# Kernel tuning notes

Measured on AMD Instinct MI355X. Metric: run time of the kernel, lower is better.

The kernel has to match this reference:

```python
import jax, jax.numpy as jnp
import numpy as np

N_NODES = 50000
N_EDGES = 600000
D = 128
L = 3


def setup_inputs() -> dict:
    key = jax.random.key(0)
    ks = jax.random.split(key, 6)
    x = jax.random.normal(ks[0], (N_NODES, D), dtype=jnp.float32)
    edge_index = jax.random.randint(ks[1], (2, N_EDGES), 0, N_NODES, dtype=jnp.int64)
    # Glorot-ish scale for 128x128 linears
    s = 1.0 / np.sqrt(D)
    W_l = jax.random.normal(ks[2], (L, D, D), dtype=jnp.float32) * s
    b_l = jnp.zeros((L, D), dtype=jnp.float32)
    W_r = jax.random.normal(ks[3], (L, D, D), dtype=jnp.float32) * s
    W_out = jax.random.normal(ks[4], (D, 1), dtype=jnp.float32) * s
    b_out = jnp.zeros((1,), dtype=jnp.float32)
    return {"x": x, "edge_index": edge_index, "W_l": W_l, "b_l": b_l,
            "W_r": W_r, "W_out": W_out, "b_out": b_out}


def reference(x, edge_index, W_l, b_l, W_r, W_out, b_out):
    # PyG SAGEConv (aggr='mean', root_weight=True):
    #   out_i = lin_l(mean_{j: (j->i)} x_j) + lin_r(x_i)
    src = edge_index[0]
    dst = edge_index[1]
    n = x.shape[0]
    deg = jax.ops.segment_sum(jnp.ones(src.shape, x.dtype), dst, num_segments=n)
    inv_deg = (1.0 / jnp.maximum(deg, 1.0))[:, None]  # [N,1]
    h = x
    for i in range(W_l.shape[0]):  # fixed small layer count
        agg = jax.ops.segment_sum(h[src], dst, num_segments=n) * inv_deg  # [N,D]
        h = agg @ W_l[i] + b_l[i] + h @ W_r[i]
        h = jax.nn.relu(h)  # dropout is identity at eval (p=0.0)
    return (h @ W_out + b_out)[:, 0]  # squeeze(-1) -> [N]
```

## Files before the change

### kernel.cpp

```cpp
#include <hip/hip_runtime.h>

#define N_NODES 50000
#define N_EDGES 600000
#define D 128
#define NLAYERS 3
#define ELL_W 64

typedef __attribute__((ext_vector_type(8))) short short8;
typedef __attribute__((ext_vector_type(4))) float floatx4;

__device__ __forceinline__ float bf_lo(unsigned u) { return __uint_as_float(u << 16); }
__device__ __forceinline__ float bf_hi(unsigned u) { return __uint_as_float(u & 0xffff0000u); }
__device__ __forceinline__ unsigned short f2bf(float f) {
    unsigned u = __float_as_uint(f);
    return (unsigned short)((u + 0x7fffu + ((u >> 16) & 1u)) >> 16);
}


#define SEC_A (N_NODES * D / 4)
#define SEC_B (SEC_A + NLAYERS * D * 256)
#define SEC_TOT (SEC_B + N_NODES)

__global__ void cvt_init_kernel(const float* __restrict__ x, const float* __restrict__ Wl,
                                const float* __restrict__ Wr,
                                unsigned short* __restrict__ xb,
                                unsigned short* __restrict__ hb1,
                                unsigned short* __restrict__ hb2,
                                unsigned short* __restrict__ WtF,
                                int* __restrict__ cursor) {
    int i = blockIdx.x * blockDim.x + threadIdx.x;
    if (i < SEC_A) {
        float4 v = ((const float4*)x)[i];
        ushort4 o;
        o.x = f2bf(v.x); o.y = f2bf(v.y); o.z = f2bf(v.z); o.w = f2bf(v.w);
        ((ushort4*)xb)[i] = o;
    } else if (i < SEC_B) {
        int t = i - SEC_A;
        int l = t >> 15;
        int r = t & 32767;
        int f = r >> 3;
        int ii = r & 7;
        int jkt = f >> 6;
        int lane = f & 63;
        int j = jkt >> 3;
        int kt = jkt & 7;
        int half = lane & 15;
        int quad = lane >> 4;
        int n = j * 16 + half;
        int k = kt * 32 + quad * 8 + ii;
        float v = (k < D) ? Wl[(size_t)l * D * D + (size_t)k * D + n]
                          : Wr[(size_t)l * D * D + (size_t)(k - D) * D + n];
        WtF[t] = f2bf(v);
    } else if (i < SEC_TOT) {
        int j = i - SEC_B;
        cursor[j] = 0;
        if (j < D) {
            xb[(size_t)N_NODES * D + j] = 0;
            hb1[(size_t)N_NODES * D + j] = 0;
            hb2[(size_t)N_NODES * D + j] = 0;
        }
    }
}


__global__ void fill_kernel(const int* __restrict__ src, const int* __restrict__ dst,
                            int* __restrict__ cursor, unsigned short* __restrict__ ell) {
    int e = blockIdx.x * blockDim.x + threadIdx.x;
    if (e < N_EDGES) {
        int d_ = dst[e];
        int pos = atomicAdd(&cursor[d_], 1);
        if (pos < ELL_W) ell[(size_t)d_ * ELL_W + pos] = (unsigned short)src[e];
    }
}


template <bool LAST>
__global__ __launch_bounds__(256) void fused_layer_kernel(
    const unsigned short* __restrict__ hin,
    const int* __restrict__ degc, const unsigned short* __restrict__ ell,
    const unsigned short* __restrict__ WtF, const float* __restrict__ bias,
    unsigned short* __restrict__ hout,
    const float* __restrict__ Wout, const float* __restrict__ bout,
    float* __restrict__ out) {
    __shared__ union {
        unsigned short a[32 * 256];
        unsigned short c[32][136];
        float red[32][4];
    } sh;

    int m0 = blockIdx.x * 32;
    int tid = threadIdx.x;

    uint4 st0, st1;
    int strow0, stcol0, strow1, stcol1;
    {
        int t0 = tid;
        strow0 = t0 >> 4; stcol0 = t0 & 15;
        int row0 = min(m0 + strow0, N_NODES - 1);
        st0 = *((const uint4*)(hin + (size_t)row0 * D + stcol0 * 8));
        int t1 = 256 + tid;
        strow1 = t1 >> 4; stcol1 = t1 & 15;
        int row1 = min(m0 + strow1, N_NODES - 1);
        st1 = *((const uint4*)(hin + (size_t)row1 * D + stcol1 * 8));
    }

    {
        int grp = tid >> 4;
        int q = tid & 15;
        int nodeA = m0 + grp;
        int nodeB = m0 + grp + 16;
        int dA = (nodeA < N_NODES) ? min(degc[nodeA], ELL_W) : 0;
        int dB = (nodeB < N_NODES) ? min(degc[nodeB], ELL_W) : 0;
        #pragma unroll
        for (int half_ = 0; half_ < 2; ++half_) {
            int nl = grp + half_ * 16;
            int node = m0 + nl;
            int d = half_ ? dB : dA;
            float a[8] = {0.f, 0.f, 0.f, 0.f, 0.f, 0.f, 0.f, 0.f};
            float b8[8] = {0.f, 0.f, 0.f, 0.f, 0.f, 0.f, 0.f, 0.f};
            float w = 0.f;
            if (node < N_NODES) {
                int pd = (d + 3) & ~3;
                int base = node * ELL_W;
                for (int e = 0; e < pd; e += 16) {
                    int cnt = min(pd - e, 16);
                    int idx = ell[base + e + q];
                    for (int j = 0; j < cnt; j += 4) {
                        int rem = d - e - j;
                        int s0 = __shfl(idx, j + 0, 16);
                        int s1 = __shfl(idx, j + 1, 16);
                        int s2 = __shfl(idx, j + 2, 16);
                        int s3 = __shfl(idx, j + 3, 16);
                        s1 = (1 < rem) ? s1 : N_NODES;
                        s2 = (2 < rem) ? s2 : N_NODES;
                        s3 = (3 < rem) ? s3 : N_NODES;
                        uint4 v0 = *((const uint4*)(hin + (size_t)s0 * D + q * 8));
                        uint4 v1 = *((const uint4*)(hin + (size_t)s1 * D + q * 8));
                        uint4 v2 = *((const uint4*)(hin + (size_t)s2 * D + q * 8));
                        uint4 v3 = *((const uint4*)(hin + (size_t)s3 * D + q * 8));
                        a[0] += bf_lo(v0.x); a[1] += bf_hi(v0.x);
                        a[2] += bf_lo(v0.y); a[3] += bf_hi(v0.y);
                        a[4] += bf_lo(v0.z); a[5] += bf_hi(v0.z);
                        a[6] += bf_lo(v0.w); a[7] += bf_hi(v0.w);
                        b8[0] += bf_lo(v1.x); b8[1] += bf_hi(v1.x);
                        b8[2] += bf_lo(v1.y); b8[3] += bf_hi(v1.y);
                        b8[4] += bf_lo(v1.z); b8[5] += bf_hi(v1.z);
                        b8[6] += bf_lo(v1.w); b8[7] += bf_hi(v1.w);
                        a[0] += bf_lo(v2.x); a[1] += bf_hi(v2.x);
                        a[2] += bf_lo(v2.y); a[3] += bf_hi(v2.y);
                        a[4] += bf_lo(v2.z); a[5] += bf_hi(v2.z);
                        a[6] += bf_lo(v2.w); a[7] += bf_hi(v2.w);
                        b8[0] += bf_lo(v3.x); b8[1] += bf_hi(v3.x);
                        b8[2] += bf_lo(v3.y); b8[3] += bf_hi(v3.y);
                        b8[4] += bf_lo(v3.z); b8[5] += bf_hi(v3.z);
                        b8[6] += bf_lo(v3.w); b8[7] += bf_hi(v3.w);
                    }
                }
                w = 1.0f / (float)max(d, 1);
            }
            uint4 o;
            o.x = (unsigned)f2bf((a[0] + b8[0]) * w) | ((unsigned)f2bf((a[1] + b8[1]) * w) << 16);
            o.y = (unsigned)f2bf((a[2] + b8[2]) * w) | ((unsigned)f2bf((a[3] + b8[3]) * w) << 16);
            o.z = (unsigned)f2bf((a[4] + b8[4]) * w) | ((unsigned)f2bf((a[5] + b8[5]) * w) << 16);
            o.w = (unsigned)f2bf((a[6] + b8[6]) * w) | ((unsigned)f2bf((a[7] + b8[7]) * w) << 16);
            int chunk = q ^ (nl & 7);
            *((uint4*)&sh.a[nl * 256 + chunk * 8]) = o;
        }
    }

    {
        int chunk0 = (16 + stcol0) ^ (strow0 & 7);
        *((uint4*)&sh.a[strow0 * 256 + chunk0 * 8]) = st0;
        int chunk1 = (16 + stcol1) ^ (strow1 & 7);
        *((uint4*)&sh.a[strow1 * 256 + chunk1 * 8]) = st1;
    }
    __syncthreads();

    int wv = tid >> 6;
    int lane = tid & 63;
    int half = lane & 15;
    int quad = lane >> 4;

    floatx4 acc[2][2];
    #pragma unroll
    for (int mt = 0; mt < 2; mt++)
        #pragma unroll
        for (int jj = 0; jj < 2; jj++)
            acc[mt][jj] = (floatx4){0.f, 0.f, 0.f, 0.f};

    const short8* Bf = (const short8*)WtF;
    #pragma unroll
    for (int kt = 0; kt < 8; kt++) {
        int ch = (kt * 4 + quad) ^ (half & 7);
        short8 a0 = *((const short8*)&sh.a[half * 256 + ch * 8]);
        short8 a1 = *((const short8*)&sh.a[(16 + half) * 256 + ch * 8]);
        #pragma unroll
        for (int jj = 0; jj < 2; jj++) {
            int j = wv * 2 + jj;
            short8 b = Bf[(j * 8 + kt) * 64 + lane];
            acc[0][jj] = __builtin_amdgcn_mfma_f32_16x16x32_bf16(a0, b, acc[0][jj], 0, 0, 0);
            acc[1][jj] = __builtin_amdgcn_mfma_f32_16x16x32_bf16(a1, b, acc[1][jj], 0, 0, 0);
        }
    }
    __syncthreads();

    if (!LAST) {
        #pragma unroll
        for (int jj = 0; jj < 2; jj++) {
            int col = (wv * 2 + jj) * 16 + half;
            float bv = bias[col];
            #pragma unroll
            for (int mt = 0; mt < 2; mt++)
                #pragma unroll
                for (int r = 0; r < 4; r++)
                    sh.c[mt * 16 + quad * 4 + r][col] = f2bf(fmaxf(acc[mt][jj][r] + bv, 0.f));
        }
        __syncthreads();
        #pragma unroll
        for (int it = 0; it < 2; ++it) {
            int t = it * 256 + tid;
            int rl = t >> 4;
            int c = t & 15;
            int row = m0 + rl;
            if (row < N_NODES)
                *((uint4*)(hout + (size_t)row * D + c * 8)) = *((const uint4*)&sh.c[rl][c * 8]);
        }
    } else {
        float vout[2][4] = {{0.f, 0.f, 0.f, 0.f}, {0.f, 0.f, 0.f, 0.f}};
        #pragma unroll
        for (int jj = 0; jj < 2; jj++) {
            int col = (wv * 2 + jj) * 16 + half;
            float bv = bias[col];
            float wo = Wout[col];
            #pragma unroll
            for (int mt = 0; mt < 2; mt++)
                #pragma unroll
                for (int r = 0; r < 4; r++)
                    vout[mt][r] += fmaxf(acc[mt][jj][r] + bv, 0.f) * wo;
        }
        #pragma unroll
        for (int off = 1; off < 16; off <<= 1) {
            #pragma unroll
            for (int mt = 0; mt < 2; mt++)
                #pragma unroll
                for (int r = 0; r < 4; r++)
                    vout[mt][r] += __shfl_xor(vout[mt][r], off, 64);
        }
        if (half == 0) {
            #pragma unroll
            for (int mt = 0; mt < 2; mt++)
                #pragma unroll
                for (int r = 0; r < 4; r++)
                    sh.red[mt * 16 + quad * 4 + r][wv] = vout[mt][r];
        }
        __syncthreads();
        if (tid < 32) {
            int row = m0 + tid;
            if (row < N_NODES)
                out[row] = sh.red[tid][0] + sh.red[tid][1] +
                           sh.red[tid][2] + sh.red[tid][3] + bout[0];
        }
    }
}


extern "C" void kernel_launch(void* const* d_in, const int* in_sizes, int n_in,
                              void* d_out, int out_size, void* d_ws, size_t ws_size,
                              hipStream_t stream) {
    const float* x     = (const float*)d_in[0];
    const int*   edge  = (const int*)d_in[1];
    const float* W_l   = (const float*)d_in[2];
    const float* b_l   = (const float*)d_in[3];
    const float* W_r   = (const float*)d_in[4];
    const float* W_out = (const float*)d_in[5];
    const float* b_out = (const float*)d_in[6];
    float* out = (float*)d_out;

    char* ws = (char*)d_ws;
    size_t off = 0;
    auto alloc = [&](size_t bytes) -> void* {
        void* p = ws + off;
        off += (bytes + 255) & ~(size_t)255;
        return p;
    };
    unsigned short* xb  = (unsigned short*)alloc((size_t)(N_NODES + 1) * D * 2);
    unsigned short* hb1 = (unsigned short*)alloc((size_t)(N_NODES + 1) * D * 2);
    unsigned short* hb2 = (unsigned short*)alloc((size_t)(N_NODES + 1) * D * 2);
    unsigned short* WtF = (unsigned short*)alloc((size_t)NLAYERS * D * 256 * 2);
    int* cursor = (int*)alloc((size_t)N_NODES * sizeof(int));
    unsigned short* ell = (unsigned short*)alloc((size_t)N_NODES * ELL_W * sizeof(unsigned short));

    const int* src = edge;
    const int* dst = edge + N_EDGES;

    cvt_init_kernel<<<(SEC_TOT + 255) / 256, 256, 0, stream>>>(
        x, W_l, W_r, xb, hb1, hb2, WtF, cursor);
    fill_kernel<<<(N_EDGES + 255) / 256, 256, 0, stream>>>(src, dst, cursor, ell);

    const int grid = (N_NODES + 31) / 32;

    fused_layer_kernel<false><<<grid, 256, 0, stream>>>(
        xb, cursor, ell, WtF, b_l, hb1, W_out, b_out, out);
    fused_layer_kernel<false><<<grid, 256, 0, stream>>>(
        hb1, cursor, ell, WtF + (size_t)1 * D * 256, b_l + 1 * D, hb2, W_out, b_out, out);
    fused_layer_kernel<true><<<grid, 256, 0, stream>>>(
        hb2, cursor, ell, WtF + (size_t)2 * D * 256, b_l + 2 * D, hb1, W_out, b_out, out);
}
```

Before: 207.4 us.

## Merge three layer launches into a persistent kernel with grid barriers

Replaces the three per-layer kernel launches with one persistent kernel of 1024 blocks. Each block loops over 32-row tiles, and the layers are separated by a software grid barrier built on atomic counters that the init kernel zeroes. The goal is to remove inter-kernel launch gaps and tail drain between layers. In exchange it adds barrier spin overhead and an uneven tile-to-block distribution. It also depends on all 1024 blocks being co-resident; if they are not, the barrier deadlocks.

```diff
diff --git a/kernel.cpp b/kernel.cpp
--- a/kernel.cpp
+++ b/kernel.cpp
@@ -5,6 +5,7 @@
 #define D 128
 #define NLAYERS 3
 #define ELL_W 64
+#define NBLK 1024
 
 typedef __attribute__((ext_vector_type(8))) short short8;
 typedef __attribute__((ext_vector_type(4))) float floatx4;
@@ -15,7 +16,6 @@
     unsigned u = __float_as_uint(f);
     return (unsigned short)((u + 0x7fffu + ((u >> 16) & 1u)) >> 16);
 }
-
 
 #define SEC_A (N_NODES * D / 4)
 #define SEC_B (SEC_A + NLAYERS * D * 256)
@@ -27,7 +27,7 @@
                                 unsigned short* __restrict__ hb1,
                                 unsigned short* __restrict__ hb2,
                                 unsigned short* __restrict__ WtF,
-                                int* __restrict__ cursor) {
+                                int* __restrict__ cursor, int* __restrict__ bar) {
     int i = blockIdx.x * blockDim.x + threadIdx.x;
     if (i < SEC_A) {
         float4 v = ((const float4*)x)[i];
@@ -54,6 +54,7 @@
     } else if (i < SEC_TOT) {
         int j = i - SEC_B;
         cursor[j] = 0;
+        if (j < 256) bar[j] = 0;
         if (j < D) {
             xb[(size_t)N_NODES * D + j] = 0;
             hb1[(size_t)N_NODES * D + j] = 0;
@@ -61,7 +62,6 @@
         }
     }
 }
-
 
 __global__ void fill_kernel(const int* __restrict__ src, const int* __restrict__ dst,
                             int* __restrict__ cursor, unsigned short* __restrict__ ell) {
@@ -73,22 +73,36 @@
     }
 }
 
+__device__ __forceinline__ void grid_barrier(int* bar, int nblk) {
+    __syncthreads();
+    if (threadIdx.x == 0) {
+        __threadfence();
+        int g = blockIdx.x & 7;
+        int v = atomicAdd(&bar[g * 16], 1) + 1;
+        if (v == (nblk >> 3)) atomicAdd(&bar[127], 1);
+        while (__hip_atomic_load(&bar[127], __ATOMIC_ACQUIRE,
+                                 __HIP_MEMORY_SCOPE_AGENT) < 8)
+            __builtin_amdgcn_s_sleep(16);
+        __threadfence();
+    }
+    __syncthreads();
+}
+
+union SharedU {
+    unsigned short a[32 * 256];
+    unsigned short c[32][136];
+    float red[32][4];
+};
 
 template <bool LAST>
-__global__ __launch_bounds__(256) void fused_layer_kernel(
+__device__ __forceinline__ void layer_tile(
+    SharedU& sh, int m0,
     const unsigned short* __restrict__ hin,
     const int* __restrict__ degc, const unsigned short* __restrict__ ell,
     const unsigned short* __restrict__ WtF, const float* __restrict__ bias,
     unsigned short* __restrict__ hout,
     const float* __restrict__ Wout, const float* __restrict__ bout,
     float* __restrict__ out) {
-    __shared__ union {
-        unsigned short a[32 * 256];
-        unsigned short c[32][136];
-        float red[32][4];
-    } sh;
-
-    int m0 = blockIdx.x * 32;
     int tid = threadIdx.x;
 
     uint4 st0, st1;
@@ -261,6 +275,29 @@
                            sh.red[tid][2] + sh.red[tid][3] + bout[0];
         }
     }
+    __syncthreads();
+}
+
+__global__ __launch_bounds__(256, 4) void persistent_layers_kernel(
+    const unsigned short* __restrict__ xb,
+    unsigned short* __restrict__ hb1, unsigned short* __restrict__ hb2,
+    const int* __restrict__ degc, const unsigned short* __restrict__ ell,
+    const unsigned short* __restrict__ WtF, const float* __restrict__ b_l,
+    const float* __restrict__ Wout, const float* __restrict__ bout,
+    float* __restrict__ out, int* __restrict__ bar) {
+    __shared__ SharedU sh;
+    const int NT = (N_NODES + 31) / 32;
+
+    for (int t = blockIdx.x; t < NT; t += gridDim.x)
+        layer_tile<false>(sh, t * 32, xb, degc, ell, WtF, b_l, hb1, Wout, bout, out);
+    grid_barrier(bar, gridDim.x);
+    for (int t = blockIdx.x; t < NT; t += gridDim.x)
+        layer_tile<false>(sh, t * 32, hb1, degc, ell, WtF + D * 256, b_l + D,
+                          hb2, Wout, bout, out);
+    grid_barrier(bar + 128, gridDim.x);
+    for (int t = blockIdx.x; t < NT; t += gridDim.x)
+        layer_tile<true>(sh, t * 32, hb2, degc, ell, WtF + 2 * D * 256, b_l + 2 * D,
+                         hb1, Wout, bout, out);
 }
 
 
@@ -289,20 +326,14 @@
     unsigned short* WtF = (unsigned short*)alloc((size_t)NLAYERS * D * 256 * 2);
     int* cursor = (int*)alloc((size_t)N_NODES * sizeof(int));
     unsigned short* ell = (unsigned short*)alloc((size_t)N_NODES * ELL_W * sizeof(unsigned short));
+    int* bar    = (int*)alloc(1024);
 
     const int* src = edge;
     const int* dst = edge + N_EDGES;
 
     cvt_init_kernel<<<(SEC_TOT + 255) / 256, 256, 0, stream>>>(
-        x, W_l, W_r, xb, hb1, hb2, WtF, cursor);
+        x, W_l, W_r, xb, hb1, hb2, WtF, cursor, bar);
     fill_kernel<<<(N_EDGES + 255) / 256, 256, 0, stream>>>(src, dst, cursor, ell);
-
-    const int grid = (N_NODES + 31) / 32;
-
-    fused_layer_kernel<false><<<grid, 256, 0, stream>>>(
-        xb, cursor, ell, WtF, b_l, hb1, W_out, b_out, out);
-    fused_layer_kernel<false><<<grid, 256, 0, stream>>>(
-        hb1, cursor, ell, WtF + (size_t)1 * D * 256, b_l + 1 * D, hb2, W_out, b_out, out);
-    fused_layer_kernel<true><<<grid, 256, 0, stream>>>(
-        hb2, cursor, ell, WtF + (size_t)2 * D * 256, b_l + 2 * D, hb1, W_out, b_out, out);
-}
+    persistent_layers_kernel<<<NBLK, 256, 0, stream>>>(
+        xb, hb1, hb2, cursor, ell, WtF, b_l, W_out, b_out, out, bar);
+}
```

Measured after the change: 750.7 us. +262.0%, slower.
